# Optimization experiments

Hardware: AMD Instinct MI355X
Metric: run time of the kernel (lower is better)

## Reference

```python
import jax, jax.numpy as jnp
import numpy as np

P = 16       # n_partitions
E = 512      # entity_dim
H = 512      # hidden_dim
N = 8192     # number of entities in the batch


def setup_inputs() -> dict:
    key = jax.random.key(0)
    ks = jax.random.split(key, 7)
    s_in = 1.0 / np.sqrt(E)
    s_h = 1.0 / np.sqrt(H)
    return {
        "e_embedding": jax.random.normal(ks[0], (N, E), dtype=jnp.float32),
        # stacked weights for the P independent SimpleMLPs (fused as batched GEMMs)
        "W0": jax.random.uniform(ks[1], (P, E, H), jnp.float32, -s_in, s_in),
        "b0": jax.random.uniform(ks[2], (P, H), jnp.float32, -s_in, s_in),
        "W1": jax.random.uniform(ks[3], (P, H, H), jnp.float32, -s_h, s_h),
        "b1": jax.random.uniform(ks[4], (P, H), jnp.float32, -s_h, s_h),
        "W2": jax.random.uniform(ks[5], (P, H, 1), jnp.float32, -s_h, s_h),
        "b2": jax.random.uniform(ks[6], (P, 1), jnp.float32, -s_h, s_h),
    }


def reference(e_embedding, W0, b0, W1, b1, W2, b2):
    # Each partition p runs SimpleMLP_p(e_embedding); fused as batched einsums.
    h = jax.nn.relu(jnp.einsum("ne,peh->pnh", e_embedding, W0) + b0[:, None, :])  # [P,N,H]
    h = jax.nn.relu(jnp.einsum("pnh,phk->pnk", h, W1) + b1[:, None, :])           # [P,N,H]
    out = jnp.einsum("pnh,pho->pno", h, W2) + b2[:, None, :]                      # [P,N,1]
    out = jax.nn.sigmoid(out)  # regularizer: fuzzy membership in [0,1]
    # torch.stack(...).squeeze().T  ->  [P,N] -> [N,P]
    return jnp.squeeze(out, axis=-1).T
```

## Files before the change

### kernel.cpp

```cpp
#include <hip/hip_runtime.h>
#include <stdint.h>

typedef _Float16 f16;
typedef _Float16 f16x8 __attribute__((ext_vector_type(8)));
typedef float floatx4 __attribute__((ext_vector_type(4)));
typedef unsigned short u16;

#define PDIM 16

__device__ __forceinline__ floatx4 mfma_16x16x32(f16x8 a, f16x8 b, floatx4 c) {
  return __builtin_amdgcn_mfma_f32_16x16x32_f16(a, b, c, 0, 0, 0);
}

__device__ __forceinline__ void stage16(const f16* g, f16* lds_base) {
  __builtin_amdgcn_global_load_lds(
      (const __attribute__((address_space(1))) void*)g,
      (__attribute__((address_space(3))) void*)lds_base, 16, 0, 0);
}

#define WAITVM3() asm volatile("s_waitcnt vmcnt(3)" ::: "memory")
#define WAITVM0() asm volatile("s_waitcnt vmcnt(0)" ::: "memory")
#define BAR()     asm volatile("s_barrier" ::: "memory")
#define SCHEDFENCE() __builtin_amdgcn_sched_barrier(0)

__device__ __forceinline__ void decode_block(int b, int nwg, int& p, int& ht,
                                             int& nt) {
  const int NT = nwg >> 6;
  if ((NT & 7) == 0) {
    const int x  = b & 7;
    const int u  = b >> 3;
    const int cg = u >> 6;
    const int i  = u & 63;
    ht = i & 3;
    const int pl  = (i >> 2) & 1;
    const int ntl = i >> 3;
    p  = x * 2 + pl;
    nt = cg * 8 + ntl;
  } else {
    p  = b & 15;
    ht = (b >> 4) & 3;
    nt = b >> 6;
  }
}


__global__ __launch_bounds__(256) void kprep(const float* __restrict__ emb,
                                             const float* __restrict__ W0,
                                             const float* __restrict__ W1,
                                             const float* __restrict__ b0,
                                             const float* __restrict__ b1,
                                             const float* __restrict__ W2,
                                             const float* __restrict__ b2,
                                             f16* __restrict__ embB,
                                             f16* __restrict__ W0T,
                                             f16* __restrict__ W1T,
                                             float* __restrict__ smallF,
                                             int n8, int nConvBlk) {
  const int b = blockIdx.x;
  const int t = threadIdx.x;
  if (b < 2048) {
    const int m  = b >> 10;
    const int p  = (b >> 6) & 15;
    const int tr = (b >> 3) & 7;
    const int tc = b & 7;
    const float* src = (m ? W1 : W0) + ((size_t)p << 18);
    f16*         dst = (m ? W1T : W0T) + ((size_t)p << 18);
    const int w = t >> 6;
    const int l = t & 63;
    const int h  = tc * 64 + l;
    const int e0 = tr * 64 + w * 16;
    const float* sp = src + (size_t)e0 * 512 + h;
    float v[16];
#pragma unroll
    for (int j = 0; j < 16; ++j) v[j] = sp[(size_t)j * 512];
    union { f16 hh[16]; uint4 u[2]; } o;
#pragma unroll
    for (int j = 0; j < 16; ++j) o.hh[j] = (f16)v[j];
    f16* dp = dst + (size_t)h * 512 + e0;
    ((uint4*)dp)[0] = o.u[0];
    ((uint4*)dp)[1] = o.u[1];
  } else if (b < 2048 + nConvBlk) {
    const int i = (b - 2048) * 256 + t;
    if (i < n8) {
      const float4* s = (const float4*)emb;
      float4 a = s[i * 2], bb = s[i * 2 + 1];
      union { f16 h[8]; uint4 v; } o;
      o.h[0] = (f16)a.x;  o.h[1] = (f16)a.y;  o.h[2] = (f16)a.z;  o.h[3] = (f16)a.w;
      o.h[4] = (f16)bb.x; o.h[5] = (f16)bb.y; o.h[6] = (f16)bb.z; o.h[7] = (f16)bb.w;
      *(uint4*)(embB + (size_t)i * 8) = o.v;
    }
  } else {
    const int j = (b - 2048 - nConvBlk) * 256 + t;
    if (j < 24592) {
      const float* src;
      int off;
      if (j < 8192)       { src = b0; off = j; }
      else if (j < 16384) { src = b1; off = j - 8192; }
      else if (j < 24576) { src = W2; off = j - 16384; }
      else                { src = b2; off = j - 24576; }
      smallF[j] = src[off];
    }
  }
}

__global__ __launch_bounds__(512) void kgemm1(const f16* __restrict__ emb,
                                              const f16* __restrict__ W0T,
                                              const float* __restrict__ small,
                                              f16* __restrict__ h0,
                                              int Nc) {
  __shared__ f16 smem[36864];
  const int b  = blockIdx.x;
  const int p  = b & 15;
  const int ht = (b >> 4) & 3;
  const int nt = b >> 6;
  const int n0 = nt * 256;
  const int hc0 = ht * 128;
  const int tid = threadIdx.x;
  const int w = tid >> 6;
  const int lane = tid & 63;
  const int q = lane >> 4;
  const int mm = lane & 15;
  const int wr = (w >> 1) * 64;
  const int wc = (w & 1) * 64;
  const int srow = lane >> 2;
  const int kch  = (((lane & 3) ^ ((lane >> 3) & 3)) * 8);
  const int qs   = (q ^ ((mm >> 1) & 3)) * 8;

  const f16* Arow = emb + (size_t)n0 * 512;
  const f16* Brow = W0T + ((size_t)p << 18) + (size_t)hc0 * 512;

  floatx4 acc[4][4];
#pragma unroll
  for (int i = 0; i < 4; ++i)
#pragma unroll
    for (int j = 0; j < 4; ++j) acc[i][j] = floatx4{0.f, 0.f, 0.f, 0.f};

  const int r0 = w * 16 + srow;
#pragma unroll
  for (int tpre = 0; tpre < 2; ++tpre) {
    const int kn = tpre * 32;
    f16* Ab = smem + tpre * 8192;
    f16* Bb = smem + 24576 + tpre * 4096;
    stage16(Arow + (size_t)r0 * 512 + kn + kch, Ab + (w * 16) * 32);
    stage16(Arow + (size_t)(128 + r0) * 512 + kn + kch, Ab + (128 + w * 16) * 32);
    stage16(Brow + (size_t)r0 * 512 + kn + kch, Bb + (w * 16) * 32);
  }

#pragma unroll
  for (int it = 0; it < 16; ++it) {
    if (it < 15) { WAITVM3(); } else { WAITVM0(); }
    BAR();
    if (it + 2 < 16) {
      const int nb = (it + 2) % 3;
      const int kn = (it + 2) * 32;
      f16* Ab = smem + nb * 8192;
      f16* Bb = smem + 24576 + nb * 4096;
      stage16(Arow + (size_t)r0 * 512 + kn + kch, Ab + (w * 16) * 32);
      stage16(Arow + (size_t)(128 + r0) * 512 + kn + kch, Ab + (128 + w * 16) * 32);
      stage16(Brow + (size_t)r0 * 512 + kn + kch, Bb + (w * 16) * 32);
    }
    const int cb = it % 3;
    const f16* A = smem + cb * 8192;
    const f16* B = smem + 24576 + cb * 4096;
    f16x8 af[4], bv[4];
#pragma unroll
    for (int rt = 0; rt < 4; ++rt)
      af[rt] = *(const f16x8*)&A[(wr + rt * 16 + mm) * 32 + qs];
#pragma unroll
    for (int ct = 0; ct < 4; ++ct)
      bv[ct] = *(const f16x8*)&B[(wc + ct * 16 + mm) * 32 + qs];
#pragma unroll
    for (int rt = 0; rt < 4; ++rt)
#pragma unroll
      for (int ct = 0; ct < 4; ++ct)
        acc[rt][ct] = mfma_16x16x32(af[rt], bv[ct], acc[rt][ct]);
    SCHEDFENCE();
  }
  SCHEDFENCE();

  __syncthreads();
  f16* Cst = smem;
#pragma unroll
  for (int pass = 0; pass < 4; ++pass) {
    if ((w >> 1) == pass) {
#pragma unroll
      for (int ct = 0; ct < 4; ++ct) {
        const float bvv = small[p * 512 + hc0 + wc + ct * 16 + mm];
#pragma unroll
        for (int rt = 0; rt < 4; ++rt)
#pragma unroll
          for (int r = 0; r < 4; ++r) {
            float v = acc[rt][ct][r] + bvv;
            v = v > 0.f ? v : 0.f;
            Cst[(rt * 16 + q * 4 + r) * 136 + wc + ct * 16 + mm] = (f16)v;
          }
      }
    }
    __syncthreads();
#pragma unroll
    for (int i = 0; i < 2; ++i) {
      const int row = (tid >> 4) + i * 32;
      const int chunk = tid & 15;
      uint4 v = *(const uint4*)&Cst[row * 136 + chunk * 8];
      *(uint4*)&h0[((size_t)p * Nc + n0 + pass * 64 + row) * 512 + hc0 +
                   chunk * 8] = v;
    }
    if (pass < 3) __syncthreads();
  }
}

__global__ __launch_bounds__(512) void kgemm2(const f16* __restrict__ h0,
                                              const f16* __restrict__ W1T,
                                              const float* __restrict__ small,
                                              float* __restrict__ pacc,
                                              int Nc) {
  __shared__ f16 smem[36864];
  __shared__ float oacc[256];
  int p, ht, nt;
  decode_block(blockIdx.x, gridDim.x, p, ht, nt);
  const int n0 = nt * 256;
  const int hc0 = ht * 128;
  const int tid = threadIdx.x;
  const int w = tid >> 6;
  const int lane = tid & 63;
  const int q = lane >> 4;
  const int mm = lane & 15;
  const int wr = (w >> 1) * 64;
  const int wc = (w & 1) * 64;
  const int srow = lane >> 2;
  const int kch = (((lane & 3) ^ ((lane >> 3) & 3)) * 8);
  const int qs  = (q ^ ((mm >> 1) & 3)) * 8;
  if (tid < 256) oacc[tid] = 0.f;

  const f16* Arow = h0 + ((size_t)p * Nc + n0) * 512;
  const f16* Brow = W1T + ((size_t)p << 18) + (size_t)hc0 * 512;

  floatx4 acc[4][4];
#pragma unroll
  for (int i = 0; i < 4; ++i)
#pragma unroll
    for (int j = 0; j < 4; ++j) acc[i][j] = floatx4{0.f, 0.f, 0.f, 0.f};

  const int r0 = w * 16 + srow;
#pragma unroll
  for (int tpre = 0; tpre < 2; ++tpre) {
    const int kn = tpre * 32;
    f16* Ab = smem + tpre * 8192;
    f16* Bb = smem + 24576 + tpre * 4096;
    stage16(Arow + (size_t)r0 * 512 + kn + kch, Ab + (w * 16) * 32);
    stage16(Arow + (size_t)(128 + r0) * 512 + kn + kch, Ab + (128 + w * 16) * 32);
    stage16(Brow + (size_t)r0 * 512 + kn + kch, Bb + (w * 16) * 32);
  }

#pragma unroll
  for (int it = 0; it < 16; ++it) {
    if (it < 15) { WAITVM3(); } else { WAITVM0(); }
    BAR();
    if (it + 2 < 16) {
      const int nb = (it + 2) % 3;
      const int kn = (it + 2) * 32;
      f16* Ab = smem + nb * 8192;
      f16* Bb = smem + 24576 + nb * 4096;
      stage16(Arow + (size_t)r0 * 512 + kn + kch, Ab + (w * 16) * 32);
      stage16(Arow + (size_t)(128 + r0) * 512 + kn + kch, Ab + (128 + w * 16) * 32);
      stage16(Brow + (size_t)r0 * 512 + kn + kch, Bb + (w * 16) * 32);
    }
    const int cb = it % 3;
    const f16* A = smem + cb * 8192;
    const f16* B = smem + 24576 + cb * 4096;
    f16x8 af[4], bv[4];
#pragma unroll
    for (int rt = 0; rt < 4; ++rt)
      af[rt] = *(const f16x8*)&A[(wr + rt * 16 + mm) * 32 + qs];
#pragma unroll
    for (int ct = 0; ct < 4; ++ct)
      bv[ct] = *(const f16x8*)&B[(wc + ct * 16 + mm) * 32 + qs];
#pragma unroll
    for (int rt = 0; rt < 4; ++rt)
#pragma unroll
      for (int ct = 0; ct < 4; ++ct)
        acc[rt][ct] = mfma_16x16x32(af[rt], bv[ct], acc[rt][ct]);
    SCHEDFENCE();
  }
  SCHEDFENCE();

  float pd[4][4];
#pragma unroll
  for (int i = 0; i < 4; ++i)
#pragma unroll
    for (int r = 0; r < 4; ++r) pd[i][r] = 0.f;
#pragma unroll
  for (int ct = 0; ct < 4; ++ct) {
    const int col = hc0 + wc + ct * 16 + mm;
    const float b1v = small[8192 + p * 512 + col];
    const float w2v = small[16384 + p * 512 + col];
#pragma unroll
    for (int rt = 0; rt < 4; ++rt)
#pragma unroll
      for (int r = 0; r < 4; ++r) {
        float v = acc[rt][ct][r] + b1v;
        v = v > 0.f ? v : 0.f;
        pd[rt][r] += v * w2v;
      }
  }
#pragma unroll
  for (int rt = 0; rt < 4; ++rt)
#pragma unroll
    for (int r = 0; r < 4; ++r) {
      float v = pd[rt][r];
      v += __shfl_xor(v, 1, 16);
      v += __shfl_xor(v, 2, 16);
      v += __shfl_xor(v, 4, 16);
      v += __shfl_xor(v, 8, 16);
      if (mm == 0) atomicAdd(&oacc[wr + rt * 16 + q * 4 + r], v);
    }
  __syncthreads();
  if (tid < 256)
    pacc[(size_t)(p * 4 + ht) * Nc + n0 + tid] = oacc[tid];
}

__global__ __launch_bounds__(256) void kfin(const float* __restrict__ pacc,
                                            const float* __restrict__ small,
                                            float* __restrict__ out, int Nc) {
  const int idx = blockIdx.x * 256 + threadIdx.x;
  if (idx >= Nc * 16) return;
  const int n = idx >> 4;
  const int p = idx & 15;
  float v = small[24576 + p];
#pragma unroll
  for (int ht = 0; ht < 4; ++ht) v += pacc[(size_t)(p * 4 + ht) * Nc + n];
  out[(size_t)n * 16 + p] = 1.f / (1.f + expf(-v));
}

__global__ __launch_bounds__(64) void knaive(const float* __restrict__ emb,
                                             const float* __restrict__ W0,
                                             const float* __restrict__ b0,
                                             const float* __restrict__ W1,
                                             const float* __restrict__ b1,
                                             const float* __restrict__ W2,
                                             const float* __restrict__ b2,
                                             float* __restrict__ out) {
  const int n = blockIdx.x >> 4;
  const int p = blockIdx.x & 15;
  __shared__ float h0s[512];
  __shared__ float h1s[512];
  const size_t wb = (size_t)p << 18;
  const int t = threadIdx.x;
  for (int h = t; h < 512; h += 64) {
    float a = 0.f;
    for (int e = 0; e < 512; ++e)
      a += emb[(size_t)n * 512 + e] * W0[wb + (size_t)e * 512 + h];
    a += b0[p * 512 + h];
    h0s[h] = a > 0.f ? a : 0.f;
  }
  __syncthreads();
  for (int k = t; k < 512; k += 64) {
    float a = 0.f;
    for (int hh = 0; hh < 512; ++hh)
      a += h0s[hh] * W1[wb + (size_t)hh * 512 + k];
    a += b1[p * 512 + k];
    h1s[k] = a > 0.f ? a : 0.f;
  }
  __syncthreads();
  float s = 0.f;
  for (int k = t; k < 512; k += 64) s += h1s[k] * W2[p * 512 + k];
  for (int off = 32; off; off >>= 1) s += __shfl_down(s, off, 64);
  if (t == 0)
    out[(size_t)n * 16 + p] = 1.f / (1.f + expf(-(s + b2[p])));
}

extern "C" void kernel_launch(void* const* d_in, const int* in_sizes, int n_in,
                              void* d_out, int out_size, void* d_ws, size_t ws_size,
                              hipStream_t stream) {
  (void)n_in; (void)out_size;
  const float* emb = (const float*)d_in[0];
  const float* W0  = (const float*)d_in[1];
  const float* b0  = (const float*)d_in[2];
  const float* W1  = (const float*)d_in[3];
  const float* b1  = (const float*)d_in[4];
  const float* W2  = (const float*)d_in[5];
  const float* b2  = (const float*)d_in[6];
  float* out = (float*)d_out;

  const int N = in_sizes[0] / 512;

  char* ws = (char*)d_ws;
  f16*   W0T    = (f16*)ws;
  f16*   W1T    = (f16*)(ws + (8ll << 20));
  float* smallF = (float*)(ws + (16ll << 20));
  float* pacc   = (float*)(ws + (16ll << 20) + 131072);
  f16*   embB   = (f16*)(ws + (16ll << 20) + 131072 + (size_t)N * 256);
  f16*   h0     = (f16*)(ws + (16ll << 20) + 131072 + (size_t)N * 256 +
                         (size_t)N * 1024);
  const long long fixed = (16ll << 20) + 131072 + (long long)N * 256 +
                          (long long)N * 1024;
  long long avail = (long long)ws_size - fixed;
  long long rows = avail > 0 ? avail / (16 * 512 * 2) : 0;
  int Nc = (int)((rows / 256) * 256);
  if (Nc > N) Nc = N;

  if (Nc < 256 || (N % 256) != 0) {
    knaive<<<dim3(N * PDIM), dim3(64), 0, stream>>>(emb, W0, b0, W1, b1, W2,
                                                    b2, out);
    return;
  }

  const int n8 = N * 512 / 8;
  const int nConvBlk = (n8 + 255) / 256;
  kprep<<<dim3(2048 + nConvBlk + 97), dim3(256), 0, stream>>>(
      emb, W0, W1, b0, b1, W2, b2, embB, W0T, W1T, smallF, n8, nConvBlk);

  for (int noff = 0; noff < N; noff += Nc) {
    const int cur = (N - noff < Nc) ? (N - noff) : Nc;
    kgemm1<<<dim3(64 * (cur / 256)), dim3(512), 0, stream>>>(
        embB + (size_t)noff * 512, W0T, smallF, h0, cur);
    kgemm2<<<dim3(64 * (cur / 256)), dim3(512), 0, stream>>>(
        h0, W1T, smallF, pacc, cur);
    kfin<<<dim3((cur * 16 + 255) / 256), dim3(256), 0, stream>>>(
        pacc, smallF, out + (size_t)noff * 16, cur);
  }
}
```

Before: 282.8 us.

## Enlarge GEMM tiles to 256x256 with quadrant-wise ping-pong pipeline and wave priority

Both GEMM kernels now compute 256x256 output tiles per workgroup instead of 256x128, halving the grid and the number of column splits in the second-layer reduction. A shared gemm_core stages 64-wide K slices into a double-buffered, XOR-swizzled LDS layout split into row/column halves and walks the four quadrants in sequence. Each quadrant step interleaves the next prefetch with its MFMAs and raises wave priority around the MFMA block. The larger tile reuses more data per LDS load but uses 128KB of LDS and more accumulator registers, which lowers occupancy and halves the workgroup count.

```diff
diff --git a/kernel.cpp b/kernel.cpp
--- a/kernel.cpp
+++ b/kernel.cpp
@@ -18,31 +18,35 @@
       (__attribute__((address_space(3))) void*)lds_base, 16, 0, 0);
 }
 
-#define WAITVM3() asm volatile("s_waitcnt vmcnt(3)" ::: "memory")
+#define WAITVM4() asm volatile("s_waitcnt vmcnt(4)" ::: "memory")
+#define WAITVM2() asm volatile("s_waitcnt vmcnt(2)" ::: "memory")
 #define WAITVM0() asm volatile("s_waitcnt vmcnt(0)" ::: "memory")
 #define BAR()     asm volatile("s_barrier" ::: "memory")
+#define LGKM0()   asm volatile("s_waitcnt lgkmcnt(0)" ::: "memory")
 #define SCHEDFENCE() __builtin_amdgcn_sched_barrier(0)
-
-__device__ __forceinline__ void decode_block(int b, int nwg, int& p, int& ht,
-                                             int& nt) {
-  const int NT = nwg >> 6;
+#define PRIO1() __builtin_amdgcn_s_setprio(1)
+#define PRIO0() __builtin_amdgcn_s_setprio(0)
+
+
+__device__ __forceinline__ void decode_block2(int b, int nwg, int& p, int& ht,
+                                              int& nt) {
+  const int NT = nwg >> 5;
   if ((NT & 7) == 0) {
     const int x  = b & 7;
     const int u  = b >> 3;
-    const int cg = u >> 6;
-    const int i  = u & 63;
-    ht = i & 3;
-    const int pl  = (i >> 2) & 1;
-    const int ntl = i >> 3;
+    const int i  = u & 31;
+    const int cg = u >> 5;
+    ht = i & 1;
+    const int pl  = (i >> 1) & 1;
+    const int ntl = i >> 2;
     p  = x * 2 + pl;
     nt = cg * 8 + ntl;
   } else {
     p  = b & 15;
-    ht = (b >> 4) & 3;
-    nt = b >> 6;
-  }
-}
-
+    ht = (b >> 4) & 1;
+    nt = b >> 5;
+  }
+}
 
 __global__ __launch_bounds__(256) void kprep(const float* __restrict__ emb,
                                              const float* __restrict__ W0,
@@ -103,109 +107,204 @@
   }
 }
 
+__device__ __forceinline__ void stageU(const f16* M, int h, int tt, f16* buf,
+                                       int w, int srow8, int kg8) {
+  stage16(M + (size_t)(h * 128 + w * 8 + srow8) * 512 + tt * 64 + kg8,
+          buf + (w * 8) * 64);
+  stage16(M + (size_t)(h * 128 + 64 + w * 8 + srow8) * 512 + tt * 64 + kg8,
+          buf + (64 + w * 8) * 64);
+}
+
+__device__ __forceinline__ void gemm_core(const f16* __restrict__ Arow,
+                                          const f16* __restrict__ Brow,
+                                          f16* smem, floatx4 (*acc)[2][2][4],
+                                          int w, int lane) {
+  const int q   = lane >> 4;
+  const int mm  = lane & 15;
+  const int mm7 = mm & 7;
+  const int qwr = (w & 3) * 32;
+  const int qwc = (w >> 2) * 64;
+  const int srow8 = lane >> 3;
+  const int kg8   = (((lane & 7) ^ ((lane >> 3) & 7)) * 8);
+
+  stageU(Arow, 0, 0, smem + 0 * 8192, w, srow8, kg8);
+  stageU(Brow, 0, 0, smem + 32768 + 0 * 8192, w, srow8, kg8);
+  stageU(Brow, 1, 0, smem + 32768 + 1 * 8192, w, srow8, kg8);
+  stageU(Arow, 1, 0, smem + 1 * 8192, w, srow8, kg8);
+
+  f16x8 af[2][2], bv[4][2];
+
+  for (int t = 0; t < 8; ++t) {
+    const int cb = t & 1;
+    const f16* Ah0 = smem + (cb * 2 + 0) * 8192;
+    const f16* Ah1 = smem + (cb * 2 + 1) * 8192;
+    const f16* Bh0 = smem + 32768 + (cb * 2 + 0) * 8192;
+    const f16* Bh1 = smem + 32768 + (cb * 2 + 1) * 8192;
+    const int nb = cb ^ 1;
+    f16* nAh0 = smem + (nb * 2 + 0) * 8192;
+    f16* nAh1 = smem + (nb * 2 + 1) * 8192;
+    f16* nBh0 = smem + 32768 + (nb * 2 + 0) * 8192;
+    f16* nBh1 = smem + 32768 + (nb * 2 + 1) * 8192;
+
+    WAITVM4();
+    BAR();
+#pragma unroll
+    for (int rt = 0; rt < 2; ++rt)
+#pragma unroll
+      for (int ks = 0; ks < 2; ++ks)
+        af[rt][ks] = *(const f16x8*)&Ah0[(qwr + rt * 16 + mm) * 64 +
+                                         (((ks * 4 + q) ^ mm7)) * 8];
+#pragma unroll
+    for (int ct = 0; ct < 4; ++ct)
+#pragma unroll
+      for (int ks = 0; ks < 2; ++ks)
+        bv[ct][ks] = *(const f16x8*)&Bh0[(qwc + ct * 16 + mm) * 64 +
+                                         (((ks * 4 + q) ^ mm7)) * 8];
+    if (t < 7) stageU(Arow, 0, t + 1, nAh0, w, srow8, kg8);
+    LGKM0();
+    PRIO1();
+#pragma unroll
+    for (int rt = 0; rt < 2; ++rt)
+#pragma unroll
+      for (int ct = 0; ct < 4; ++ct)
+#pragma unroll
+        for (int ks = 0; ks < 2; ++ks)
+          acc[0][0][rt][ct] = mfma_16x16x32(af[rt][ks], bv[ct][ks],
+                                            acc[0][0][rt][ct]);
+    PRIO0();
+    SCHEDFENCE();
+
+    if (t < 7) { WAITVM4(); } else { WAITVM2(); }
+    BAR();
+#pragma unroll
+    for (int ct = 0; ct < 4; ++ct)
+#pragma unroll
+      for (int ks = 0; ks < 2; ++ks)
+        bv[ct][ks] = *(const f16x8*)&Bh1[(qwc + ct * 16 + mm) * 64 +
+                                         (((ks * 4 + q) ^ mm7)) * 8];
+    if (t < 7) stageU(Brow, 0, t + 1, nBh0, w, srow8, kg8);
+    LGKM0();
+    PRIO1();
+#pragma unroll
+    for (int rt = 0; rt < 2; ++rt)
+#pragma unroll
+      for (int ct = 0; ct < 4; ++ct)
+#pragma unroll
+        for (int ks = 0; ks < 2; ++ks)
+          acc[0][1][rt][ct] = mfma_16x16x32(af[rt][ks], bv[ct][ks],
+                                            acc[0][1][rt][ct]);
+    PRIO0();
+    SCHEDFENCE();
+
+    if (t < 7) { WAITVM4(); } else { WAITVM0(); }
+    BAR();
+#pragma unroll
+    for (int rt = 0; rt < 2; ++rt)
+#pragma unroll
+      for (int ks = 0; ks < 2; ++ks)
+        af[rt][ks] = *(const f16x8*)&Ah1[(qwr + rt * 16 + mm) * 64 +
+                                         (((ks * 4 + q) ^ mm7)) * 8];
+    if (t < 7) stageU(Brow, 1, t + 1, nBh1, w, srow8, kg8);
+    LGKM0();
+    PRIO1();
+#pragma unroll
+    for (int rt = 0; rt < 2; ++rt)
+#pragma unroll
+      for (int ct = 0; ct < 4; ++ct)
+#pragma unroll
+        for (int ks = 0; ks < 2; ++ks)
+          acc[1][1][rt][ct] = mfma_16x16x32(af[rt][ks], bv[ct][ks],
+                                            acc[1][1][rt][ct]);
+    PRIO0();
+    SCHEDFENCE();
+
+    BAR();
+#pragma unroll
+    for (int ct = 0; ct < 4; ++ct)
+#pragma unroll
+      for (int ks = 0; ks < 2; ++ks)
+        bv[ct][ks] = *(const f16x8*)&Bh0[(qwc + ct * 16 + mm) * 64 +
+                                         (((ks * 4 + q) ^ mm7)) * 8];
+    if (t < 7) stageU(Arow, 1, t + 1, nAh1, w, srow8, kg8);
+    LGKM0();
+    PRIO1();
+#pragma unroll
+    for (int rt = 0; rt < 2; ++rt)
+#pragma unroll
+      for (int ct = 0; ct < 4; ++ct)
+#pragma unroll
+        for (int ks = 0; ks < 2; ++ks)
+          acc[1][0][rt][ct] = mfma_16x16x32(af[rt][ks], bv[ct][ks],
+                                            acc[1][0][rt][ct]);
+    PRIO0();
+    SCHEDFENCE();
+  }
+}
+
 __global__ __launch_bounds__(512) void kgemm1(const f16* __restrict__ emb,
                                               const f16* __restrict__ W0T,
                                               const float* __restrict__ small,
                                               f16* __restrict__ h0,
                                               int Nc) {
-  __shared__ f16 smem[36864];
+  __shared__ f16 smem[65536];
   const int b  = blockIdx.x;
   const int p  = b & 15;
-  const int ht = (b >> 4) & 3;
-  const int nt = b >> 6;
+  const int ht = (b >> 4) & 1;
+  const int nt = b >> 5;
   const int n0 = nt * 256;
-  const int hc0 = ht * 128;
+  const int hc0 = ht * 256;
   const int tid = threadIdx.x;
   const int w = tid >> 6;
   const int lane = tid & 63;
   const int q = lane >> 4;
   const int mm = lane & 15;
-  const int wr = (w >> 1) * 64;
-  const int wc = (w & 1) * 64;
-  const int srow = lane >> 2;
-  const int kch  = (((lane & 3) ^ ((lane >> 3) & 3)) * 8);
-  const int qs   = (q ^ ((mm >> 1) & 3)) * 8;
 
   const f16* Arow = emb + (size_t)n0 * 512;
   const f16* Brow = W0T + ((size_t)p << 18) + (size_t)hc0 * 512;
 
-  floatx4 acc[4][4];
-#pragma unroll
-  for (int i = 0; i < 4; ++i)
-#pragma unroll
-    for (int j = 0; j < 4; ++j) acc[i][j] = floatx4{0.f, 0.f, 0.f, 0.f};
-
-  const int r0 = w * 16 + srow;
-#pragma unroll
-  for (int tpre = 0; tpre < 2; ++tpre) {
-    const int kn = tpre * 32;
-    f16* Ab = smem + tpre * 8192;
-    f16* Bb = smem + 24576 + tpre * 4096;
-    stage16(Arow + (size_t)r0 * 512 + kn + kch, Ab + (w * 16) * 32);
-    stage16(Arow + (size_t)(128 + r0) * 512 + kn + kch, Ab + (128 + w * 16) * 32);
-    stage16(Brow + (size_t)r0 * 512 + kn + kch, Bb + (w * 16) * 32);
-  }
-
-#pragma unroll
-  for (int it = 0; it < 16; ++it) {
-    if (it < 15) { WAITVM3(); } else { WAITVM0(); }
-    BAR();
-    if (it + 2 < 16) {
-      const int nb = (it + 2) % 3;
-      const int kn = (it + 2) * 32;
-      f16* Ab = smem + nb * 8192;
-      f16* Bb = smem + 24576 + nb * 4096;
-      stage16(Arow + (size_t)r0 * 512 + kn + kch, Ab + (w * 16) * 32);
-      stage16(Arow + (size_t)(128 + r0) * 512 + kn + kch, Ab + (128 + w * 16) * 32);
-      stage16(Brow + (size_t)r0 * 512 + kn + kch, Bb + (w * 16) * 32);
-    }
-    const int cb = it % 3;
-    const f16* A = smem + cb * 8192;
-    const f16* B = smem + 24576 + cb * 4096;
-    f16x8 af[4], bv[4];
-#pragma unroll
-    for (int rt = 0; rt < 4; ++rt)
-      af[rt] = *(const f16x8*)&A[(wr + rt * 16 + mm) * 32 + qs];
-#pragma unroll
-    for (int ct = 0; ct < 4; ++ct)
-      bv[ct] = *(const f16x8*)&B[(wc + ct * 16 + mm) * 32 + qs];
-#pragma unroll
-    for (int rt = 0; rt < 4; ++rt)
-#pragma unroll
-      for (int ct = 0; ct < 4; ++ct)
-        acc[rt][ct] = mfma_16x16x32(af[rt], bv[ct], acc[rt][ct]);
-    SCHEDFENCE();
-  }
-  SCHEDFENCE();
+  floatx4 acc[2][2][2][4];
+#pragma unroll
+  for (int i = 0; i < 2; ++i)
+#pragma unroll
+    for (int j = 0; j < 2; ++j)
+#pragma unroll
+      for (int k = 0; k < 2; ++k)
+#pragma unroll
+        for (int l = 0; l < 4; ++l) acc[i][j][k][l] = floatx4{0.f, 0.f, 0.f, 0.f};
+
+  gemm_core(Arow, Brow, smem, acc, w, lane);
 
   __syncthreads();
   f16* Cst = smem;
 #pragma unroll
-  for (int pass = 0; pass < 4; ++pass) {
-    if ((w >> 1) == pass) {
-#pragma unroll
-      for (int ct = 0; ct < 4; ++ct) {
-        const float bvv = small[p * 512 + hc0 + wc + ct * 16 + mm];
-#pragma unroll
-        for (int rt = 0; rt < 4; ++rt)
-#pragma unroll
-          for (int r = 0; r < 4; ++r) {
-            float v = acc[rt][ct][r] + bvv;
-            v = v > 0.f ? v : 0.f;
-            Cst[(rt * 16 + q * 4 + r) * 136 + wc + ct * 16 + mm] = (f16)v;
-          }
-      }
+  for (int P = 0; P < 4; ++P) {
+    if (((w & 3) >> 1) == (P & 1)) {
+#pragma unroll
+      for (int qn = 0; qn < 2; ++qn)
+#pragma unroll
+        for (int ct = 0; ct < 4; ++ct) {
+          const int col = qn * 128 + (w >> 2) * 64 + ct * 16 + mm;
+          const float bvv = small[p * 512 + hc0 + col];
+#pragma unroll
+          for (int rt = 0; rt < 2; ++rt)
+#pragma unroll
+            for (int r = 0; r < 4; ++r) {
+              float v = acc[P >> 1][qn][rt][ct][r] + bvv;
+              v = v > 0.f ? v : 0.f;
+              Cst[((w & 1) * 32 + rt * 16 + q * 4 + r) * 264 + col] = (f16)v;
+            }
+        }
     }
     __syncthreads();
 #pragma unroll
-    for (int i = 0; i < 2; ++i) {
-      const int row = (tid >> 4) + i * 32;
-      const int chunk = tid & 15;
-      uint4 v = *(const uint4*)&Cst[row * 136 + chunk * 8];
-      *(uint4*)&h0[((size_t)p * Nc + n0 + pass * 64 + row) * 512 + hc0 +
-                   chunk * 8] = v;
+    for (int k = 0; k < 4; ++k) {
+      const int idx = tid + k * 512;
+      const int row = idx >> 5;
+      const int ch  = idx & 31;
+      uint4 v = *(const uint4*)&Cst[row * 264 + ch * 8];
+      *(uint4*)&h0[((size_t)p * Nc + n0 + P * 64 + row) * 512 + hc0 + ch * 8] = v;
     }
-    if (pass < 3) __syncthreads();
+    if (P < 3) __syncthreads();
   }
 }
 
@@ -214,109 +313,74 @@
                                               const float* __restrict__ small,
                                               float* __restrict__ pacc,
                                               int Nc) {
-  __shared__ f16 smem[36864];
+  __shared__ f16 smem[65536];
   __shared__ float oacc[256];
   int p, ht, nt;
-  decode_block(blockIdx.x, gridDim.x, p, ht, nt);
+  decode_block2(blockIdx.x, gridDim.x, p, ht, nt);
   const int n0 = nt * 256;
-  const int hc0 = ht * 128;
+  const int hc0 = ht * 256;
   const int tid = threadIdx.x;
   const int w = tid >> 6;
   const int lane = tid & 63;
   const int q = lane >> 4;
   const int mm = lane & 15;
-  const int wr = (w >> 1) * 64;
-  const int wc = (w & 1) * 64;
-  const int srow = lane >> 2;
-  const int kch = (((lane & 3) ^ ((lane >> 3) & 3)) * 8);
-  const int qs  = (q ^ ((mm >> 1) & 3)) * 8;
   if (tid < 256) oacc[tid] = 0.f;
 
   const f16* Arow = h0 + ((size_t)p * Nc + n0) * 512;
   const f16* Brow = W1T + ((size_t)p << 18) + (size_t)hc0 * 512;
 
-  floatx4 acc[4][4];
-#pragma unroll
-  for (int i = 0; i < 4; ++i)
-#pragma unroll
-    for (int j = 0; j < 4; ++j) acc[i][j] = floatx4{0.f, 0.f, 0.f, 0.f};
-
-  const int r0 = w * 16 + srow;
-#pragma unroll
-  for (int tpre = 0; tpre < 2; ++tpre) {
-    const int kn = tpre * 32;
-    f16* Ab = smem + tpre * 8192;
-    f16* Bb = smem + 24576 + tpre * 4096;
-    stage16(Arow + (size_t)r0 * 512 + kn + kch, Ab + (w * 16) * 32);
-    stage16(Arow + (size_t)(128 + r0) * 512 + kn + kch, Ab + (128 + w * 16) * 32);
-    stage16(Brow + (size_t)r0 * 512 + kn + kch, Bb + (w * 16) * 32);
-  }
-
-#pragma unroll
-  for (int it = 0; it < 16; ++it) {
-    if (it < 15) { WAITVM3(); } else { WAITVM0(); }
-    BAR();
-    if (it + 2 < 16) {
-      const int nb = (it + 2) % 3;
-      const int kn = (it + 2) * 32;
-      f16* Ab = smem + nb * 8192;
-      f16* Bb = smem + 24576 + nb * 4096;
-      stage16(Arow + (size_t)r0 * 512 + kn + kch, Ab + (w * 16) * 32);
-      stage16(Arow + (size_t)(128 + r0) * 512 + kn + kch, Ab + (128 + w * 16) * 32);
-      stage16(Brow + (size_t)r0 * 512 + kn + kch, Bb + (w * 16) * 32);
-    }
-    const int cb = it % 3;
-    const f16* A = smem + cb * 8192;
-    const f16* B = smem + 24576 + cb * 4096;
-    f16x8 af[4], bv[4];
-#pragma unroll
-    for (int rt = 0; rt < 4; ++rt)
-      af[rt] = *(const f16x8*)&A[(wr + rt * 16 + mm) * 32 + qs];
-#pragma unroll
-    for (int ct = 0; ct < 4; ++ct)
-      bv[ct] = *(const f16x8*)&B[(wc + ct * 16 + mm) * 32 + qs];
-#pragma unroll
-    for (int rt = 0; rt < 4; ++rt)
-#pragma unroll
-      for (int ct = 0; ct < 4; ++ct)
-        acc[rt][ct] = mfma_16x16x32(af[rt], bv[ct], acc[rt][ct]);
-    SCHEDFENCE();
-  }
-  SCHEDFENCE();
-
-  float pd[4][4];
-#pragma unroll
-  for (int i = 0; i < 4; ++i)
-#pragma unroll
-    for (int r = 0; r < 4; ++r) pd[i][r] = 0.f;
-#pragma unroll
-  for (int ct = 0; ct < 4; ++ct) {
-    const int col = hc0 + wc + ct * 16 + mm;
-    const float b1v = small[8192 + p * 512 + col];
-    const float w2v = small[16384 + p * 512 + col];
-#pragma unroll
-    for (int rt = 0; rt < 4; ++rt)
+  floatx4 acc[2][2][2][4];
+#pragma unroll
+  for (int i = 0; i < 2; ++i)
+#pragma unroll
+    for (int j = 0; j < 2; ++j)
+#pragma unroll
+      for (int k = 0; k < 2; ++k)
+#pragma unroll
+        for (int l = 0; l < 4; ++l) acc[i][j][k][l] = floatx4{0.f, 0.f, 0.f, 0.f};
+
+  gemm_core(Arow, Brow, smem, acc, w, lane);
+
+  __syncthreads();
+#pragma unroll
+  for (int qm = 0; qm < 2; ++qm) {
+    float pd[2][4];
+#pragma unroll
+    for (int rt = 0; rt < 2; ++rt)
+#pragma unroll
+      for (int r = 0; r < 4; ++r) pd[rt][r] = 0.f;
+#pragma unroll
+    for (int qn = 0; qn < 2; ++qn)
+#pragma unroll
+      for (int ct = 0; ct < 4; ++ct) {
+        const int col = hc0 + qn * 128 + (w >> 2) * 64 + ct * 16 + mm;
+        const float b1v = small[8192 + p * 512 + col];
+        const float w2v = small[16384 + p * 512 + col];
+#pragma unroll
+        for (int rt = 0; rt < 2; ++rt)
+#pragma unroll
+          for (int r = 0; r < 4; ++r) {
+            float v = acc[qm][qn][rt][ct][r] + b1v;
+            v = v > 0.f ? v : 0.f;
+            pd[rt][r] += v * w2v;
+          }
+      }
+#pragma unroll
+    for (int rt = 0; rt < 2; ++rt)
 #pragma unroll
       for (int r = 0; r < 4; ++r) {
-        float v = acc[rt][ct][r] + b1v;
-        v = v > 0.f ? v : 0.f;
-        pd[rt][r] += v * w2v;
+        float v = pd[rt][r];
+        v += __shfl_xor(v, 1, 16);
+        v += __shfl_xor(v, 2, 16);
+        v += __shfl_xor(v, 4, 16);
+        v += __shfl_xor(v, 8, 16);
+        if (mm == 0)
+          atomicAdd(&oacc[qm * 128 + (w & 3) * 32 + rt * 16 + q * 4 + r], v);
       }
   }
-#pragma unroll
-  for (int rt = 0; rt < 4; ++rt)
-#pragma unroll
-    for (int r = 0; r < 4; ++r) {
-      float v = pd[rt][r];
-      v += __shfl_xor(v, 1, 16);
-      v += __shfl_xor(v, 2, 16);
-      v += __shfl_xor(v, 4, 16);
-      v += __shfl_xor(v, 8, 16);
-      if (mm == 0) atomicAdd(&oacc[wr + rt * 16 + q * 4 + r], v);
-    }
   __syncthreads();
   if (tid < 256)
-    pacc[(size_t)(p * 4 + ht) * Nc + n0 + tid] = oacc[tid];
+    pacc[(size_t)(p * 2 + ht) * Nc + n0 + tid] = oacc[tid];
 }
 
 __global__ __launch_bounds__(256) void kfin(const float* __restrict__ pacc,
@@ -328,7 +392,7 @@
   const int p = idx & 15;
   float v = small[24576 + p];
 #pragma unroll
-  for (int ht = 0; ht < 4; ++ht) v += pacc[(size_t)(p * 4 + ht) * Nc + n];
+  for (int ht = 0; ht < 2; ++ht) v += pacc[(size_t)(p * 2 + ht) * Nc + n];
   out[(size_t)n * 16 + p] = 1.f / (1.f + expf(-v));
 }
 
@@ -412,9 +476,9 @@
 
   for (int noff = 0; noff < N; noff += Nc) {
     const int cur = (N - noff < Nc) ? (N - noff) : Nc;
-    kgemm1<<<dim3(64 * (cur / 256)), dim3(512), 0, stream>>>(
+    kgemm1<<<dim3(32 * (cur / 256)), dim3(512), 0, stream>>>(
         embB + (size_t)noff * 512, W0T, smallF, h0, cur);
-    kgemm2<<<dim3(64 * (cur / 256)), dim3(512), 0, stream>>>(
+    kgemm2<<<dim3(32 * (cur / 256)), dim3(512), 0, stream>>>(
         h0, W1T, smallF, pacc, cur);
     kfin<<<dim3((cur * 16 + 255) / 256), dim3(256), 0, stream>>>(
         pacc, smallF, out + (size_t)noff * 16, cur);
```

After: 247.3 us. -12.6%, faster.
